# Kernel optimization log

Measured on AMD Instinct MI355X. Metric: run time of the kernel, lower is better.

## Reference

```python
import jax, jax.numpy as jnp
import numpy as np

N_NODES = 100000
N_EDGES = 3200000
OUT_FEATURES = 128


def setup_inputs() -> dict:
    key = jax.random.key(0)
    k1, k2, k3, k4, k5 = jax.random.split(key, 5)
    edge_row = jax.random.randint(k1, (N_EDGES,), 0, N_NODES, dtype=jnp.int32)
    edge_col = jax.random.randint(k2, (N_EDGES,), 0, N_NODES, dtype=jnp.int32)
    edge_val = jax.random.uniform(k3, (N_EDGES,), dtype=jnp.float32)
    stdv = 1.0 / np.sqrt(OUT_FEATURES)
    weight = jax.random.uniform(k4, (N_NODES, OUT_FEATURES), minval=-stdv, maxval=stdv, dtype=jnp.float32)
    bias = jax.random.uniform(k5, (OUT_FEATURES,), minval=-stdv, maxval=stdv, dtype=jnp.float32)
    return {"edge_row": edge_row, "edge_col": edge_col, "edge_val": edge_val,
            "weight": weight, "bias": bias}


def reference(edge_row, edge_col, edge_val, weight, bias):
    # SpMM: out = adj @ weight, adj given in COO (row, col, val), shape [N, N]
    n_nodes = weight.shape[0]
    gathered = edge_val[:, None] * weight[edge_col]            # [E, F]
    out = jax.ops.segment_sum(gathered, edge_row, num_segments=n_nodes)  # [N, F]
    return out + bias
```

## Files before the change

### kernel.cpp

```cpp
#include <hip/hip_runtime.h>

#define F 128
#define RB 64
#define RB_SHIFT 6
#define CAP 4096
#define SCH 4096
#define PT3 512
#define EPT3 (SCH / PT3)
#define NSEG 8
#define COL_BITS 17
#define COL_MASK 0x1FFFF
#define MAXNB 2048

__global__ __launch_bounds__(256) void cvt_chist_kernel(
    const float2* __restrict__ w2, ushort* __restrict__ wq, float* __restrict__ scales,
    int n_nodes, const int* __restrict__ rows, int* __restrict__ cntmat, int n_edges,
    int nb, int nchunks) {
    if ((int)blockIdx.x < nchunks) {
        __shared__ int h[MAXNB];
        int c = blockIdx.x, t = threadIdx.x;
        for (int i = t; i < nb; i += 256) h[i] = 0;
        __syncthreads();
        int e0 = c * SCH, e1 = min(e0 + SCH, n_edges);
        for (int e = e0 + t; e < e1; e += 256) atomicAdd(&h[rows[e] >> RB_SHIFT], 1);
        __syncthreads();
        for (int i = t; i < nb; i += 256) cntmat[(size_t)c * nb + i] = h[i];
    } else {
        int row = (blockIdx.x - nchunks) * 4 + (threadIdx.x >> 6);
        if (row >= n_nodes) return;
        int lane = threadIdx.x & 63;
        float2 f = w2[(size_t)row * 64 + lane];
        float m = fmaxf(fabsf(f.x), fabsf(f.y));
        for (int off = 32; off; off >>= 1) m = fmaxf(m, __shfl_xor(m, off));
        float inv = m > 0.f ? 127.f / m : 0.f;
        int q0 = (int)rintf(f.x * inv);
        int q1 = (int)rintf(f.y * inv);
        wq[(size_t)row * 64 + lane] = (ushort)((q0 & 0xFF) | ((q1 & 0xFF) << 8));
        if (lane == 0) scales[row] = m * (1.f / 127.f);
    }
}

__global__ __launch_bounds__(256) void scanA_kernel(int* __restrict__ cntmat,
                                                    int* __restrict__ segsum,
                                                    int nb, int nchunks) {
    int b = blockIdx.x * 256 + threadIdx.x;
    if (b >= nb) return;
    int sg = blockIdx.y;
    int cps = (nchunks + NSEG - 1) / NSEG;
    int c0 = sg * cps, c1 = min(c0 + cps, nchunks);
    int run = 0;
#pragma unroll 4
    for (int c = c0; c < c1; c++) {
        int v = cntmat[(size_t)c * nb + b];
        cntmat[(size_t)c * nb + b] = run;
        run += v;
    }
    segsum[sg * nb + b] = run;
}

__global__ void scanBC_kernel(int* __restrict__ segsum, int* __restrict__ boffs, int nb) {
    __shared__ int lds[1024];
    int t = threadIdx.x;
    int per = (nb + 1023) / 1024;
    int base = t * per;
    int cnt[2] = {0, 0};
    int s = 0;
    for (int i = 0; i < per && i < 2; i++) {
        int b = base + i;
        int run = 0;
        if (b < nb) {
            for (int sg = 0; sg < NSEG; sg++) {
                int v = segsum[sg * nb + b];
                segsum[sg * nb + b] = run;
                run += v;
            }
        }
        cnt[i] = run;
        s += run;
    }
    lds[t] = s;
    __syncthreads();
    for (int off = 1; off < 1024; off <<= 1) {
        int a = (t >= off) ? lds[t - off] : 0;
        __syncthreads();
        lds[t] += a;
        __syncthreads();
    }
    int excl = lds[t] - s;
    for (int i = 0; i < per && i < 2; i++) {
        int b = base + i;
        if (b < nb) {
            boffs[b] = excl;
            excl += cnt[i];
        }
    }
    if (t == 1023) boffs[nb] = lds[1023];
}

__global__ __launch_bounds__(PT3) void scatter_kernel(
    const int* __restrict__ rows, const int* __restrict__ cols,
    const float* __restrict__ vals, const float* __restrict__ scales,
    const int* __restrict__ boffs, const int* __restrict__ segsum,
    const int* __restrict__ cntmat, int2* __restrict__ epk, int n_edges, int nb,
    int nchunks) {
    __shared__ int relc[MAXNB];
    __shared__ int hist[MAXNB];
    __shared__ int lcur[MAXNB];
    __shared__ int2 buf[SCH];
    __shared__ int sidx[SCH];
    __shared__ int wsum[PT3 / 64], wbase[PT3 / 64];
    int t = threadIdx.x;
    int lane = t & 63, w = t >> 6;
    int cps = (nchunks + NSEG - 1) / NSEG;
    int c = blockIdx.x;

    int e0 = c * SCH, e1 = min(e0 + SCH, n_edges);
    int cnt = e1 - e0;
    int sg = c / cps;

    for (int i = t; i < nb; i += PT3) {
        relc[i] = boffs[i] + segsum[sg * nb + i] + cntmat[(size_t)c * nb + i];
        hist[i] = 0;
    }
    __syncthreads();

    int er[EPT3], ec[EPT3];
    float ev[EPT3];
#pragma unroll
    for (int k = 0; k < EPT3; k++) {
        int e = e0 + t + k * PT3;
        if (e < e1) {
            er[k] = rows[e];
            ec[k] = cols[e];
            ev[k] = vals[e] * scales[ec[k]];
            atomicAdd(&hist[er[k] >> RB_SHIFT], 1);
        }
    }
    __syncthreads();

    int b0 = t << 2;
    int h0 = (b0 + 0 < nb) ? hist[b0 + 0] : 0;
    int h1 = (b0 + 1 < nb) ? hist[b0 + 1] : 0;
    int h2 = (b0 + 2 < nb) ? hist[b0 + 2] : 0;
    int h3 = (b0 + 3 < nb) ? hist[b0 + 3] : 0;
    int psum = h0 + h1 + h2 + h3;
    int v = psum;
#pragma unroll
    for (int off = 1; off < 64; off <<= 1) {
        int a = __shfl_up(v, off);
        if (lane >= off) v += a;
    }
    if (lane == 63) wsum[w] = v;
    __syncthreads();
    if (t == 0) {
        int run = 0;
        for (int i = 0; i < PT3 / 64; i++) {
            wbase[i] = run;
            run += wsum[i];
        }
    }
    __syncthreads();
    int excl = v - psum + wbase[w];
    if (b0 + 0 < nb) { lcur[b0 + 0] = excl; relc[b0 + 0] -= excl; }
    excl += h0;
    if (b0 + 1 < nb) { lcur[b0 + 1] = excl; relc[b0 + 1] -= excl; }
    excl += h1;
    if (b0 + 2 < nb) { lcur[b0 + 2] = excl; relc[b0 + 2] -= excl; }
    excl += h2;
    if (b0 + 3 < nb) { lcur[b0 + 3] = excl; relc[b0 + 3] -= excl; }
    __syncthreads();

#pragma unroll
    for (int k = 0; k < EPT3; k++) {
        int e = e0 + t + k * PT3;
        if (e < e1) {
            int b = er[k] >> RB_SHIFT;
            int p = atomicAdd(&lcur[b], 1);
            buf[p] = make_int2(ec[k] | ((er[k] & (RB - 1)) << COL_BITS),
                               __float_as_int(ev[k]));
            sidx[p] = relc[b] + p;
        }
    }
    __syncthreads();

    for (int i = t; i < cnt; i += PT3) epk[sidx[i]] = buf[i];
}

__global__ __launch_bounds__(512, 8) void sortacc_kernel(
    const int* __restrict__ boffs, const int2* __restrict__ epk,
    const ushort* __restrict__ wq, const float* __restrict__ bias,
    float* __restrict__ out, int n_nodes) {
    __shared__ int2 buf[CAP];
    __shared__ int hist[RB], lstart[RB], lcur[RB];
    int b = blockIdx.x;
    int s = boffs[b];
    int cnt = boffs[b + 1] - s;
    int row0 = b << RB_SHIFT;
    int t = threadIdx.x;
    int lane = t & 63, w = t >> 6;
    float2 bb = ((const float2*)bias)[lane];

#define DEQX(u) ((float)(int)(signed char)((u) & 0xFF))
#define DEQY(u) ((float)((int)(short)(u) >> 8))
#define WOFF(px) ((((uint)(px) & COL_MASK) << 6) | (uint)lane)

    if (cnt <= CAP) {
        if (t < RB) hist[t] = 0;
        __syncthreads();
        int2 r0, r1, r2, r3, r4, r5, r6, r7;
#define LOADK(rk, k)                                                     \
        {                                                                \
            int i = t + (k)*512;                                         \
            if (i < cnt) {                                               \
                rk = epk[s + i];                                         \
                atomicAdd(&hist[(unsigned)rk.x >> COL_BITS], 1);         \
            }                                                            \
        }
        LOADK(r0, 0) LOADK(r1, 1) LOADK(r2, 2) LOADK(r3, 3)
        LOADK(r4, 4) LOADK(r5, 5) LOADK(r6, 6) LOADK(r7, 7)
#undef LOADK
        __syncthreads();
        if (w == 0) {
            int hv = hist[lane];
            int v = hv;
#pragma unroll
            for (int off = 1; off < 64; off <<= 1) {
                int a = __shfl_up(v, off);
                if (lane >= off) v += a;
            }
            lstart[lane] = v - hv;
            lcur[lane] = v - hv;
        }
        __syncthreads();
#define SCATK(rk, k)                                                         \
        {                                                                    \
            int i = t + (k)*512;                                             \
            if (i < cnt) {                                                   \
                int p = atomicAdd(&lcur[(unsigned)rk.x >> COL_BITS], 1);     \
                buf[p] = make_int2((int)(((uint)rk.x & COL_MASK) << 6), rk.y);\
            }                                                                \
        }
        SCATK(r0, 0) SCATK(r1, 1) SCATK(r2, 2) SCATK(r3, 3)
        SCATK(r4, 4) SCATK(r5, 5) SCATK(r6, 6) SCATK(r7, 7)
#undef SCATK
        __syncthreads();

        for (int j = 0; j < 8; j++) {
            int rl = w * 8 + j;
            int gr = row0 + rl;
            if (gr >= n_nodes) break;
            int e = lstart[rl];
            int end = e + hist[rl];
            float ax = 0.f, ay = 0.f;
            for (; e + 12 <= end; e += 12) {
                int2 p0 = buf[e],     p1 = buf[e + 1], p2 = buf[e + 2];
                int2 p3 = buf[e + 3], p4 = buf[e + 4], p5 = buf[e + 5];
                int2 p6 = buf[e + 6], p7 = buf[e + 7], p8 = buf[e + 8];
                int2 p9 = buf[e + 9], pa = buf[e + 10], pb = buf[e + 11];
                uint u0 = wq[(uint)p0.x + lane];
                uint u1 = wq[(uint)p1.x + lane];
                uint u2 = wq[(uint)p2.x + lane];
                uint u3 = wq[(uint)p3.x + lane];
                uint u4 = wq[(uint)p4.x + lane];
                uint u5 = wq[(uint)p5.x + lane];
                uint u6 = wq[(uint)p6.x + lane];
                uint u7 = wq[(uint)p7.x + lane];
                uint u8 = wq[(uint)p8.x + lane];
                uint u9 = wq[(uint)p9.x + lane];
                uint ua = wq[(uint)pa.x + lane];
                uint ub = wq[(uint)pb.x + lane];
                float v0 = __int_as_float(p0.y), v1 = __int_as_float(p1.y);
                float v2 = __int_as_float(p2.y), v3 = __int_as_float(p3.y);
                float v4 = __int_as_float(p4.y), v5 = __int_as_float(p5.y);
                float v6 = __int_as_float(p6.y), v7 = __int_as_float(p7.y);
                float v8 = __int_as_float(p8.y), v9 = __int_as_float(p9.y);
                float va = __int_as_float(pa.y), vb = __int_as_float(pb.y);
                ax += v0 * DEQX(u0) + v1 * DEQX(u1) + v2 * DEQX(u2) + v3 * DEQX(u3) +
                      v4 * DEQX(u4) + v5 * DEQX(u5) + v6 * DEQX(u6) + v7 * DEQX(u7) +
                      v8 * DEQX(u8) + v9 * DEQX(u9) + va * DEQX(ua) + vb * DEQX(ub);
                ay += v0 * DEQY(u0) + v1 * DEQY(u1) + v2 * DEQY(u2) + v3 * DEQY(u3) +
                      v4 * DEQY(u4) + v5 * DEQY(u5) + v6 * DEQY(u6) + v7 * DEQY(u7) +
                      v8 * DEQY(u8) + v9 * DEQY(u9) + va * DEQY(ua) + vb * DEQY(ub);
            }
            for (; e + 4 <= end; e += 4) {
                int2 p0 = buf[e], p1 = buf[e + 1], p2 = buf[e + 2], p3 = buf[e + 3];
                uint u0 = wq[(uint)p0.x + lane];
                uint u1 = wq[(uint)p1.x + lane];
                uint u2 = wq[(uint)p2.x + lane];
                uint u3 = wq[(uint)p3.x + lane];
                float v0 = __int_as_float(p0.y), v1 = __int_as_float(p1.y);
                float v2 = __int_as_float(p2.y), v3 = __int_as_float(p3.y);
                ax += v0 * DEQX(u0) + v1 * DEQX(u1) + v2 * DEQX(u2) + v3 * DEQX(u3);
                ay += v0 * DEQY(u0) + v1 * DEQY(u1) + v2 * DEQY(u2) + v3 * DEQY(u3);
            }
            for (; e < end; ++e) {
                int2 pk = buf[e];
                uint u = wq[(uint)pk.x + lane];
                float v = __int_as_float(pk.y);
                ax += v * DEQX(u);
                ay += v * DEQY(u);
            }
            ((float2*)(out + (size_t)gr * F))[lane] = make_float2(ax + bb.x, ay + bb.y);
        }
    } else {
        for (int j = 0; j < 8; j++) {
            int rl = w * 8 + j;
            int gr = row0 + rl;
            if (gr >= n_nodes) break;
            float ax = 0.f, ay = 0.f;
            for (int e = s; e < s + cnt; ++e) {
                int2 pk = epk[e];
                if ((int)((unsigned)pk.x >> COL_BITS) == rl) {
                    uint u = wq[WOFF(pk.x)];
                    float v = __int_as_float(pk.y);
                    ax += v * DEQX(u);
                    ay += v * DEQY(u);
                }
            }
            ((float2*)(out + (size_t)gr * F))[lane] = make_float2(ax + bb.x, ay + bb.y);
        }
    }
#undef DEQX
#undef DEQY
#undef WOFF
}

__global__ void init_out_kernel(float* __restrict__ out, const float* __restrict__ bias,
                                int n_nodes) {
    const float4* b4 = (const float4*)bias;
    float4* o4 = (float4*)out;
    int total = n_nodes * (F / 4);
    for (int i = blockIdx.x * blockDim.x + threadIdx.x; i < total;
         i += gridDim.x * blockDim.x)
        o4[i] = b4[i & (F / 4 - 1)];
}

__global__ void edge_scatter_kernel(const int* __restrict__ rows,
                                    const int* __restrict__ cols,
                                    const float* __restrict__ vals,
                                    const float* __restrict__ weight,
                                    float* __restrict__ out, int n_edges) {
    int e = (blockIdx.x * blockDim.x + threadIdx.x) >> 6;
    if (e >= n_edges) return;
    int lane = threadIdx.x & 63;
    float2 w = ((const float2*)(weight + (size_t)cols[e] * F))[lane];
    float val = vals[e];
    float* o = out + (size_t)rows[e] * F + lane * 2;
    unsafeAtomicAdd(o, val * w.x);
    unsafeAtomicAdd(o + 1, val * w.y);
}

extern "C" void kernel_launch(void* const* d_in, const int* in_sizes, int n_in,
                              void* d_out, int out_size, void* d_ws, size_t ws_size,
                              hipStream_t stream) {
    const int*   rows   = (const int*)d_in[0];
    const int*   cols   = (const int*)d_in[1];
    const float* vals   = (const float*)d_in[2];
    const float* weight = (const float*)d_in[3];
    const float* bias   = (const float*)d_in[4];
    float* out = (float*)d_out;

    int n_edges = in_sizes[0];
    int n_nodes = out_size / F;
    int nb = (n_nodes + RB - 1) / RB;
    int nchunks = (n_edges + SCH - 1) / SCH;

    size_t head_ints  = ((size_t)nb + 2) & ~(size_t)1;
    size_t epk_off    = head_ints * 4;
    size_t scales_off = epk_off + (size_t)n_edges * 8;
    size_t wq_off     = (scales_off + (size_t)n_nodes * 4 + 255) & ~(size_t)255;
    size_t mat_off    = (wq_off + (size_t)n_nodes * F + 255) & ~(size_t)255;
    size_t seg_off    = mat_off + (size_t)nchunks * nb * 4;
    size_t need       = seg_off + (size_t)NSEG * nb * 4;

    if (ws_size < need || n_nodes > (1 << COL_BITS) || nb > MAXNB) {
        init_out_kernel<<<2048, 256, 0, stream>>>(out, bias, n_nodes);
        int grid = (n_edges + 3) / 4;
        edge_scatter_kernel<<<grid, 256, 0, stream>>>(rows, cols, vals, weight, out,
                                                      n_edges);
        return;
    }

    int* boffs    = (int*)d_ws;
    int2* epk     = (int2*)((char*)d_ws + epk_off);
    float* scales = (float*)((char*)d_ws + scales_off);
    ushort* wq    = (ushort*)((char*)d_ws + wq_off);
    int* cntmat   = (int*)((char*)d_ws + mat_off);
    int* segsum   = (int*)((char*)d_ws + seg_off);

    int cvt_blocks = (n_nodes + 3) / 4;
    cvt_chist_kernel<<<nchunks + cvt_blocks, 256, 0, stream>>>(
        (const float2*)weight, wq, scales, n_nodes, rows, cntmat, n_edges, nb, nchunks);
    dim3 ga((nb + 255) / 256, NSEG);
    scanA_kernel<<<ga, 256, 0, stream>>>(cntmat, segsum, nb, nchunks);
    scanBC_kernel<<<1, 1024, 0, stream>>>(segsum, boffs, nb);
    scatter_kernel<<<nchunks, PT3, 0, stream>>>(rows, cols, vals, scales, boffs, segsum,
                                                cntmat, epk, n_edges, nb, nchunks);
    sortacc_kernel<<<nb, 512, 0, stream>>>(boffs, epk, wq, bias, out, n_nodes);
}
```

Before: 149.5 us.

## Vectorize preprocessing loads and shrink scatter shared memory with bucket ids

The weight quantization now has each thread handle four floats via float4, with a 32-lane shuffle reduction per row and packed 32-bit stores. Row histogramming uses int4 loads. The scatter kernel moves to 1024 threads, each loading four contiguous edges with vector loads, so each thread covers two buckets in the scan. It also stores a 16-bit bucket id per slot instead of a 32-bit destination index, which cuts shared memory. The aim is fewer memory transactions in the preprocessing stages, at the cost of a larger block size that may limit occupancy or scheduling.

```diff
diff --git a/kernel.cpp b/kernel.cpp
--- a/kernel.cpp
+++ b/kernel.cpp
@@ -5,7 +5,7 @@
 #define RB_SHIFT 6
 #define CAP 4096
 #define SCH 4096
-#define PT3 512
+#define PT3 1024
 #define EPT3 (SCH / PT3)
 #define NSEG 8
 #define COL_BITS 17
@@ -13,8 +13,8 @@
 #define MAXNB 2048
 
 __global__ __launch_bounds__(256) void cvt_chist_kernel(
-    const float2* __restrict__ w2, ushort* __restrict__ wq, float* __restrict__ scales,
-    int n_nodes, const int* __restrict__ rows, int* __restrict__ cntmat, int n_edges,
+    const float4* __restrict__ w4, uint* __restrict__ wq32, float* __restrict__ scales,
+    int total4, const int* __restrict__ rows, int* __restrict__ cntmat, int n_edges,
     int nb, int nchunks) {
     if ((int)blockIdx.x < nchunks) {
         __shared__ int h[MAXNB];
@@ -22,21 +22,36 @@
         for (int i = t; i < nb; i += 256) h[i] = 0;
         __syncthreads();
         int e0 = c * SCH, e1 = min(e0 + SCH, n_edges);
-        for (int e = e0 + t; e < e1; e += 256) atomicAdd(&h[rows[e] >> RB_SHIFT], 1);
+        if (e1 - e0 == SCH) {
+            const int4* r4 = (const int4*)(rows + e0);
+#pragma unroll
+            for (int k = 0; k < 4; k++) {
+                int4 rv = r4[k * 256 + t];
+                atomicAdd(&h[rv.x >> RB_SHIFT], 1);
+                atomicAdd(&h[rv.y >> RB_SHIFT], 1);
+                atomicAdd(&h[rv.z >> RB_SHIFT], 1);
+                atomicAdd(&h[rv.w >> RB_SHIFT], 1);
+            }
+        } else {
+            for (int e = e0 + t; e < e1; e += 256) atomicAdd(&h[rows[e] >> RB_SHIFT], 1);
+        }
         __syncthreads();
         for (int i = t; i < nb; i += 256) cntmat[(size_t)c * nb + i] = h[i];
     } else {
-        int row = (blockIdx.x - nchunks) * 4 + (threadIdx.x >> 6);
-        if (row >= n_nodes) return;
-        int lane = threadIdx.x & 63;
-        float2 f = w2[(size_t)row * 64 + lane];
-        float m = fmaxf(fabsf(f.x), fabsf(f.y));
-        for (int off = 32; off; off >>= 1) m = fmaxf(m, __shfl_xor(m, off));
+        int idx = (blockIdx.x - nchunks) * 256 + threadIdx.x;
+        if (idx >= total4) return;
+        float4 f = w4[idx];
+        float m = fmaxf(fmaxf(fabsf(f.x), fabsf(f.y)), fmaxf(fabsf(f.z), fabsf(f.w)));
+#pragma unroll
+        for (int off = 1; off <= 16; off <<= 1) m = fmaxf(m, __shfl_xor(m, off));
         float inv = m > 0.f ? 127.f / m : 0.f;
         int q0 = (int)rintf(f.x * inv);
         int q1 = (int)rintf(f.y * inv);
-        wq[(size_t)row * 64 + lane] = (ushort)((q0 & 0xFF) | ((q1 & 0xFF) << 8));
-        if (lane == 0) scales[row] = m * (1.f / 127.f);
+        int q2 = (int)rintf(f.z * inv);
+        int q3 = (int)rintf(f.w * inv);
+        wq32[idx] = (q0 & 0xFF) | ((q1 & 0xFF) << 8) | ((q2 & 0xFF) << 16) |
+                    ((q3 & 0xFF) << 24);
+        if ((idx & 31) == 0) scales[idx >> 5] = m * (1.f / 127.f);
     }
 }
 
@@ -107,7 +122,7 @@
     __shared__ int hist[MAXNB];
     __shared__ int lcur[MAXNB];
     __shared__ int2 buf[SCH];
-    __shared__ int sidx[SCH];
+    __shared__ ushort sbkt[SCH];
     __shared__ int wsum[PT3 / 64], wbase[PT3 / 64];
     int t = threadIdx.x;
     int lane = t & 63, w = t >> 6;
@@ -126,24 +141,37 @@
 
     int er[EPT3], ec[EPT3];
     float ev[EPT3];
-#pragma unroll
-    for (int k = 0; k < EPT3; k++) {
-        int e = e0 + t + k * PT3;
-        if (e < e1) {
-            er[k] = rows[e];
-            ec[k] = cols[e];
-            ev[k] = vals[e] * scales[ec[k]];
-            atomicAdd(&hist[er[k] >> RB_SHIFT], 1);
-        }
-    }
-    __syncthreads();
-
-    int b0 = t << 2;
+    int eb = e0 + (t << 2);
+    if (eb + 4 <= e1) {
+        int4 rv = *(const int4*)(rows + eb);
+        int4 cv = *(const int4*)(cols + eb);
+        float4 vv = *(const float4*)(vals + eb);
+        er[0] = rv.x; er[1] = rv.y; er[2] = rv.z; er[3] = rv.w;
+        ec[0] = cv.x; ec[1] = cv.y; ec[2] = cv.z; ec[3] = cv.w;
+        ev[0] = vv.x * scales[ec[0]];
+        ev[1] = vv.y * scales[ec[1]];
+        ev[2] = vv.z * scales[ec[2]];
+        ev[3] = vv.w * scales[ec[3]];
+#pragma unroll
+        for (int k = 0; k < 4; k++) atomicAdd(&hist[er[k] >> RB_SHIFT], 1);
+    } else {
+#pragma unroll
+        for (int k = 0; k < 4; k++) {
+            int e = eb + k;
+            if (e < e1) {
+                er[k] = rows[e];
+                ec[k] = cols[e];
+                ev[k] = vals[e] * scales[ec[k]];
+                atomicAdd(&hist[er[k] >> RB_SHIFT], 1);
+            }
+        }
+    }
+    __syncthreads();
+
+    int b0 = t << 1;
     int h0 = (b0 + 0 < nb) ? hist[b0 + 0] : 0;
     int h1 = (b0 + 1 < nb) ? hist[b0 + 1] : 0;
-    int h2 = (b0 + 2 < nb) ? hist[b0 + 2] : 0;
-    int h3 = (b0 + 3 < nb) ? hist[b0 + 3] : 0;
-    int psum = h0 + h1 + h2 + h3;
+    int psum = h0 + h1;
     int v = psum;
 #pragma unroll
     for (int off = 1; off < 64; off <<= 1) {
@@ -164,26 +192,22 @@
     if (b0 + 0 < nb) { lcur[b0 + 0] = excl; relc[b0 + 0] -= excl; }
     excl += h0;
     if (b0 + 1 < nb) { lcur[b0 + 1] = excl; relc[b0 + 1] -= excl; }
-    excl += h1;
-    if (b0 + 2 < nb) { lcur[b0 + 2] = excl; relc[b0 + 2] -= excl; }
-    excl += h2;
-    if (b0 + 3 < nb) { lcur[b0 + 3] = excl; relc[b0 + 3] -= excl; }
     __syncthreads();
 
 #pragma unroll
     for (int k = 0; k < EPT3; k++) {
-        int e = e0 + t + k * PT3;
+        int e = eb + k;
         if (e < e1) {
             int b = er[k] >> RB_SHIFT;
             int p = atomicAdd(&lcur[b], 1);
             buf[p] = make_int2(ec[k] | ((er[k] & (RB - 1)) << COL_BITS),
                                __float_as_int(ev[k]));
-            sidx[p] = relc[b] + p;
-        }
-    }
-    __syncthreads();
-
-    for (int i = t; i < cnt; i += PT3) epk[sidx[i]] = buf[i];
+            sbkt[p] = (ushort)b;
+        }
+    }
+    __syncthreads();
+
+    for (int i = t; i < cnt; i += PT3) epk[relc[sbkt[i]] + i] = buf[i];
 }
 
 __global__ __launch_bounds__(512, 8) void sortacc_kernel(
@@ -388,9 +412,11 @@
     int* cntmat   = (int*)((char*)d_ws + mat_off);
     int* segsum   = (int*)((char*)d_ws + seg_off);
 
-    int cvt_blocks = (n_nodes + 3) / 4;
+    int total4 = n_nodes * (F / 4);
+    int cvt_blocks = (total4 + 255) / 256;
     cvt_chist_kernel<<<nchunks + cvt_blocks, 256, 0, stream>>>(
-        (const float2*)weight, wq, scales, n_nodes, rows, cntmat, n_edges, nb, nchunks);
+        (const float4*)weight, (uint*)wq, scales, total4, rows, cntmat, n_edges, nb,
+        nchunks);
     dim3 ga((nb + 255) / 256, NSEG);
     scanA_kernel<<<ga, 256, 0, stream>>>(cntmat, segsum, nb, nchunks);
     scanBC_kernel<<<1, 1024, 0, stream>>>(segsum, boffs, nb);
```

After: 145.7 us. 2.6% less time.
